# Performance work log

Measured on AMD Instinct MI355X. Metric: run time of the kernel, lower is better.

## Reference

```python
import jax, jax.numpy as jnp
import numpy as np

HIDDEN = 2048
N_HEADS = 16
N_KV_HEADS = 4
HEAD_DIM = 128
GROUPS = N_HEADS // N_KV_HEADS
MAX_SEQ = 2048
EPS = 1e-6
ROTARY_DIM = int(HEAD_DIM * 0.5)  # partial_rotary_factor = 0.5
ROPE_THETA = 10000.0


def _rms_norm(x, w):
    xf = x.astype(jnp.float32)
    normed = xf * jax.lax.rsqrt(jnp.mean(xf * xf, axis=-1, keepdims=True) + EPS)
    return (normed * (1.0 + w.astype(jnp.float32))).astype(x.dtype)


def _apply_rotary(x, cos, sin):
    half = x.shape[-1] // 2
    x1, x2 = x[..., :half], x[..., half:]
    return jnp.concatenate([x1 * cos - x2 * sin, x2 * cos + x1 * sin], axis=-1)


def setup_inputs() -> dict:
    key = jax.random.key(0)
    ks = jax.random.split(key, 6)
    s = 0.02
    return {
        "x": jax.random.normal(ks[0], (1, MAX_SEQ, HIDDEN), jnp.float32),
        "input_pos": jnp.arange(MAX_SEQ, dtype=jnp.int32),
        "wq": jax.random.normal(ks[1], (HIDDEN, N_HEADS * HEAD_DIM * 2), jnp.float32) * s,
        "wk": jax.random.normal(ks[2], (HIDDEN, N_KV_HEADS * HEAD_DIM), jnp.float32) * s,
        "wv": jax.random.normal(ks[3], (HIDDEN, N_KV_HEADS * HEAD_DIM), jnp.float32) * s,
        "wo": jax.random.normal(ks[4], (N_HEADS * HEAD_DIM, HIDDEN), jnp.float32) * s,
        "q_norm_w": jnp.zeros((HEAD_DIM,), jnp.float32),
        "k_norm_w": jnp.zeros((HEAD_DIM,), jnp.float32),
    }


def reference(x, input_pos, wq, wk, wv, wo, q_norm_w, k_norm_w):
    B, T, _ = x.shape
    dtype = x.dtype

    qg = (x @ wq).reshape(B, T, N_HEADS, HEAD_DIM * 2)
    q, gate = qg[..., :HEAD_DIM], qg[..., HEAD_DIM:]
    k = (x @ wk).reshape(B, T, N_KV_HEADS, HEAD_DIM)
    v = (x @ wv).reshape(B, T, N_KV_HEADS, HEAD_DIM)

    q = _rms_norm(q, q_norm_w)
    k = _rms_norm(k, k_norm_w)

    # partial RoPE on the first ROTARY_DIM channels of each head
    inv_freq = 1.0 / ROPE_THETA ** (
        jnp.arange(0, ROTARY_DIM, 2, dtype=jnp.float32) / ROTARY_DIM)
    freqs = jnp.outer(input_pos.astype(jnp.float32), inv_freq)  # [T, rd/2]
    cos = jnp.cos(freqs)[:, None, :]  # [T,1,rd/2] broadcast over heads
    sin = jnp.sin(freqs)[:, None, :]
    q = jnp.concatenate(
        [_apply_rotary(q[..., :ROTARY_DIM], cos, sin), q[..., ROTARY_DIM:]], axis=-1)
    k = jnp.concatenate(
        [_apply_rotary(k[..., :ROTARY_DIM], cos, sin), k[..., ROTARY_DIM:]], axis=-1)

    q = q.astype(dtype).transpose(0, 2, 1, 3)  # [B,H,T,D]
    k = k.astype(dtype).transpose(0, 2, 1, 3)  # [B,Hkv,T,D]
    v = v.transpose(0, 2, 1, 3)

    # KV-cache scatter update (cache starts at zeros)
    kc = jnp.zeros((1, N_KV_HEADS, MAX_SEQ, HEAD_DIM), dtype).at[:, :, input_pos].set(k)
    vc = jnp.zeros((1, N_KV_HEADS, MAX_SEQ, HEAD_DIM), dtype).at[:, :, input_pos].set(v)

    # GQA: group query heads instead of materializing repeated K/V
    qg_ = q.reshape(B, N_KV_HEADS, GROUPS, T, HEAD_DIM)
    scale = 1.0 / jnp.sqrt(jnp.asarray(HEAD_DIM, dtype))
    scores = jnp.einsum("bhgtd,bhsd->bhgts", qg_, kc) * scale  # [B,Hkv,G,T,S]

    mask = jnp.tril(jnp.ones((MAX_SEQ, MAX_SEQ), bool))[input_pos]  # [T,S]
    scores = jnp.where(mask[None, None, None], scores, jnp.finfo(scores.dtype).min)
    probs = jax.nn.softmax(scores, axis=-1)

    y = jnp.einsum("bhgts,bhsd->bhgtd", probs, vc)  # [B,Hkv,G,T,D]
    y = y.reshape(B, N_HEADS, T, HEAD_DIM).transpose(0, 2, 1, 3).reshape(B, T, -1)

    y = y * jax.nn.sigmoid(gate.reshape(B, T, -1))
    return y @ wo
```

## Files before the change

kernel.cpp:

```cpp
#include <hip/hip_runtime.h>
#include <cstdint>
#include <cmath>

using u16 = unsigned short;
typedef __attribute__((ext_vector_type(4))) short s16x4;
typedef __attribute__((ext_vector_type(8))) short s16x8;
typedef __attribute__((ext_vector_type(8))) __bf16 bf16x8;
typedef __attribute__((ext_vector_type(4))) float f32x4;

static __device__ __forceinline__ float b2f(u16 u) {
    unsigned int x = ((unsigned int)u) << 16;
    float f; __builtin_memcpy(&f, &x, 4); return f;
}
static __device__ __forceinline__ u16 f2b(float f) {
    unsigned int x; __builtin_memcpy(&x, &f, 4);
    x += 0x7FFFu + ((x >> 16) & 1u);
    return (u16)(x >> 16);
}
static __device__ __forceinline__ bf16x8 as_bf(s16x8 s) {
    return __builtin_bit_cast(bf16x8, s);
}

static __device__ __forceinline__ void stage16(const u16* g, u16* lds_base, int lane) {
#if __has_builtin(__builtin_amdgcn_global_load_lds)
    __builtin_amdgcn_global_load_lds((const __attribute__((address_space(1))) void*)g,
                                     (__attribute__((address_space(3))) void*)lds_base,
                                     16, 0, 0);
#else
    *(s16x8*)(lds_base + (size_t)lane * 8) = *(const s16x8*)g;
#endif
}

__global__ __launch_bounds__(256) void k_wtrans(const float* __restrict__ in,
                                                u16* __restrict__ out,
                                                int K, int N) {
    __shared__ u16 tile[64][72];
    int nb = blockIdx.x * 64, kb = blockIdx.y * 64;
    int tid = threadIdx.x;
    int kr = tid >> 2, c0 = (tid & 3) * 16;
#pragma unroll
    for (int i = 0; i < 4; ++i) {
        f32x4 v = *(const f32x4*)(in + (size_t)(kb + kr) * N + nb + c0 + i * 4);
        s16x4 b;
        for (int j = 0; j < 4; ++j) b[j] = (short)f2b(v[j]);
        *(s16x4*)&tile[kr][c0 + i * 4] = b;
    }
    __syncthreads();
    int nr = tid >> 2, k0 = (tid & 3) * 16;
    s16x8 v0, v1;
    for (int j = 0; j < 8; ++j) { v0[j] = (short)tile[k0 + j][nr]; v1[j] = (short)tile[k0 + 8 + j][nr]; }
    *(s16x8*)(out + (size_t)(nb + nr) * K + kb + k0) = v0;
    *(s16x8*)(out + (size_t)(nb + nr) * K + kb + k0 + 8) = v1;
}

__global__ __launch_bounds__(256) void k_xcvt(const float* __restrict__ in,
                                              u16* __restrict__ out, int n4) {
    int i = blockIdx.x * 256 + threadIdx.x;
    int stride = gridDim.x * 256;
    for (; i < n4; i += stride) {
        f32x4 v = ((const f32x4*)in)[i];
        s16x4 b;
        for (int j = 0; j < 4; ++j) b[j] = (short)f2b(v[j]);
        ((s16x4*)out)[i] = b;
    }
}

template <bool OUT_F32>
__global__ __launch_bounds__(256) void k_gemm_bt(const u16* __restrict__ A,
                                                 const u16* __restrict__ Bt,
                                                 void* __restrict__ Cv,
                                                 int M, int N, int K) {
    __shared__ u16 As[128 * 64];
    __shared__ u16 Bs[128 * 64];
    int nx = gridDim.x, nwg = nx * gridDim.y;
    int flat = blockIdx.y * nx + blockIdx.x;
    int q = nwg >> 3, r = nwg & 7;
    int xcd = flat & 7, idx = flat >> 3;
    int wgid = (xcd < r ? xcd * (q + 1) : r * (q + 1) + (xcd - r) * q) + idx;
    int bn = (wgid % nx) * 128, bm = (wgid / nx) * 128;

    int tid = threadIdx.x, wid = tid >> 6, lane = tid & 63;
    int l15 = lane & 15, g = lane >> 4;
    int wr = (wid >> 1) * 64, wc = (wid & 1) * 64;
    f32x4 acc[4][4];
    for (int i = 0; i < 4; ++i) for (int j = 0; j < 4; ++j) acc[i][j] = f32x4{0.f, 0.f, 0.f, 0.f};

    int srow = lane >> 3;
    int scol = ((lane & 7) * 8) ^ (srow << 3);
    const u16* pa = A + (size_t)(bm + srow) * K + scol;
    const u16* pb = Bt + (size_t)(bn + srow) * K + scol;

    for (int kb = 0; kb < K; kb += 64) {
        __syncthreads();
#pragma unroll
        for (int it = 0; it < 4; ++it) {
            int c = it * 4 + wid;
            stage16(pa + (size_t)(c * 8) * K + kb, &As[c * 512], lane);
            stage16(pb + (size_t)(c * 8) * K + kb, &Bs[c * 512], lane);
        }
        __syncthreads();
        int swz = (l15 & 7) << 4;
#pragma unroll
        for (int kk = 0; kk < 64; kk += 32) {
            bf16x8 af[4], bfr[4];
            for (int mi = 0; mi < 4; ++mi) {
                const char* rp = (const char*)As + (wr + mi * 16 + l15) * 128;
                af[mi] = as_bf(*(const s16x8*)(rp + ((kk * 2 + g * 16) ^ swz)));
            }
            for (int ni = 0; ni < 4; ++ni) {
                const char* rp = (const char*)Bs + (wc + ni * 16 + l15) * 128;
                bfr[ni] = as_bf(*(const s16x8*)(rp + ((kk * 2 + g * 16) ^ swz)));
            }
            for (int mi = 0; mi < 4; ++mi)
                for (int ni = 0; ni < 4; ++ni)
                    acc[mi][ni] = __builtin_amdgcn_mfma_f32_16x16x32_bf16(af[mi], bfr[ni], acc[mi][ni], 0, 0, 0);
        }
    }
    for (int mi = 0; mi < 4; ++mi)
        for (int ni = 0; ni < 4; ++ni) {
            int row = bm + wr + mi * 16 + g * 4;
            int col = bn + wc + ni * 16 + l15;
            for (int rr = 0; rr < 4; ++rr) {
                if (OUT_F32)
                    ((float*)Cv)[(size_t)(row + rr) * N + col] = acc[mi][ni][rr];
                else
                    ((u16*)Cv)[(size_t)(row + rr) * N + col] = f2b(acc[mi][ni][rr]);
            }
        }
}

__global__ __launch_bounds__(256) void k_normrope(u16* __restrict__ qkv,
                                                  const float* __restrict__ qw,
                                                  const float* __restrict__ kw,
                                                  const int* __restrict__ pos) {
    int t = blockIdx.x;
    int tid = threadIdx.x, w = tid >> 6, l = tid & 63;
    float fp = (float)pos[t];
    int j = l & 31;
    float invf = __expf(-(float)j * (9.210340371976184f / 32.f));
    float sv, cv;
    sincosf(fp * invf, &sv, &cv);
    for (int task = w; task < 20; task += 4) {
        u16* p; const float* ww;
        if (task < 16) { p = qkv + (size_t)t * 5120 + task * 256; ww = qw; }
        else           { p = qkv + (size_t)t * 5120 + 4096 + (task - 16) * 128; ww = kw; }
        float v0 = b2f(p[l]), v1 = b2f(p[l + 64]);
        float ss = v0 * v0 + v1 * v1;
        for (int m = 32; m; m >>= 1) ss += __shfl_xor(ss, m);
        float rn = rsqrtf(ss * (1.f / 128.f) + 1e-6f);
        float q0 = v0 * rn * (1.f + ww[l]);
        float q1 = v1 * rn * (1.f + ww[l + 64]);
        float other = __shfl_xor(q0, 32);
        float ro = (l < 32) ? (q0 * cv - other * sv) : (q0 * cv + other * sv);
        p[l] = f2b(ro);
        p[l + 64] = f2b(q1);
    }
}

__global__ __launch_bounds__(256) void k_vtrans(const u16* __restrict__ qkv,
                                                u16* __restrict__ vT) {
    __shared__ u16 tile[64][136];
    int tb = blockIdx.x * 64, kvh = blockIdx.y;
    int tid = threadIdx.x;
    int tr = tid >> 2, c0 = (tid & 3) * 32;
    const u16* src = qkv + (size_t)(tb + tr) * 5120 + 4608 + kvh * 128 + c0;
#pragma unroll
    for (int i = 0; i < 4; ++i)
        *(s16x8*)&tile[tr][c0 + i * 8] = *(const s16x8*)(src + i * 8);
    __syncthreads();
    int d = tid >> 1, t0 = (tid & 1) * 32;
    u16* dst = vT + ((size_t)kvh * 128 + d) * 2048 + tb + t0;
#pragma unroll
    for (int i = 0; i < 4; ++i) {
        s16x8 v;
        for (int j = 0; j < 8; ++j) v[j] = (short)tile[t0 + i * 8 + j][d];
        *(s16x8*)(dst + i * 8) = v;
    }
}

__global__ __launch_bounds__(256) void k_attn_split(const u16* __restrict__ qkv,
                                                    const u16* __restrict__ vT,
                                                    u16* __restrict__ po,
                                                    float* __restrict__ pl) {
    __shared__ u16 Kl[64 * 128];
    __shared__ u16 Vt[128][72];
    __shared__ u16 Pl[4][16][72];
    int head = blockIdx.y, kvh = head >> 2;
    int p = blockIdx.x >> 1, hf = blockIdx.x & 1;
    int tid = threadIdx.x, wid = tid >> 6, lane = tid & 63;
    int l15 = lane & 15, g = lane >> 4;

    for (int sub = 0; sub < 2; ++sub) {
        int qt = sub ? (31 - p) : p;
        int qb0 = qt * 64;
        int nk_all = qt + 1;
        int split = (nk_all + 1) >> 1;
        int ktb = hf ? split : 0;
        int kte = hf ? nk_all : split;

        bf16x8 qf[4];
        {
            const u16* qp = qkv + (size_t)(qb0 + wid * 16 + l15) * 5120 + head * 256 + g * 8;
            for (int c = 0; c < 4; ++c) qf[c] = as_bf(*(const s16x8*)(qp + c * 32));
        }
        f32x4 oacc[8];
        for (int nb = 0; nb < 8; ++nb) oacc[nb] = f32x4{0.f, 0.f, 0.f, 0.f};
        float lsum[4] = {0.f, 0.f, 0.f, 0.f};

        for (int kt = ktb; kt < kte; ++kt) {
            int k0 = kt * 64;
            __syncthreads();
            {
#pragma unroll
                for (int i = 0; i < 4; ++i) {
                    int c = (wid << 2) | i;
                    int srow = (c << 2) + (lane >> 4);
                    int bofs = (((lane & 15) << 4) ^ ((srow & 7) << 4));
                    const u16* gs = (const u16*)((const char*)(qkv + (size_t)(k0 + srow) * 5120
                                                               + 4096 + kvh * 128) + bofs);
                    stage16(gs, &Kl[c * 512], lane);
                }
                int vr = tid >> 1, vc0 = (tid & 1) * 32;
                const u16* vs = vT + ((size_t)kvh * 128 + vr) * 2048 + k0 + vc0;
#pragma unroll
                for (int c = 0; c < 4; ++c)
                    *(s16x8*)&Vt[vr][vc0 + 8 * c] = *(const s16x8*)(vs + 8 * c);
            }
            __syncthreads();

            f32x4 sc4[4];
            for (int h2 = 0; h2 < 4; ++h2) sc4[h2] = f32x4{0.f, 0.f, 0.f, 0.f};
            for (int h2 = 0; h2 < 4; ++h2) {
                int krow = h2 * 16 + l15;
                const char* kb_ = (const char*)Kl + krow * 256;
                int sw = (krow & 7) << 4;
                for (int c = 0; c < 4; ++c) {
                    bf16x8 kf = as_bf(*(const s16x8*)(kb_ + ((c * 64 + g * 16) ^ sw)));
                    sc4[h2] = __builtin_amdgcn_mfma_f32_16x16x32_bf16(qf[c], kf, sc4[h2], 0, 0, 0);
                }
            }
            const float scale = 0.08838834764831845f;
            for (int r = 0; r < 4; ++r) {
                int tq = qb0 + wid * 16 + g * 4 + r;
                float prs = 0.f;
                for (int h2 = 0; h2 < 4; ++h2) {
                    bool msk = (k0 + h2 * 16 + l15) > tq;
                    float pv = msk ? 0.f : __expf(sc4[h2][r] * scale);
                    prs += pv;
                    Pl[wid][g * 4 + r][h2 * 16 + l15] = f2b(pv);
                }
                lsum[r] += prs;
            }
            for (int kc = 0; kc < 2; ++kc) {
                bf16x8 pa = as_bf(*(const s16x8*)&Pl[wid][l15][kc * 32 + g * 8]);
                for (int nb = 0; nb < 8; ++nb) {
                    bf16x8 vb = as_bf(*(const s16x8*)&Vt[nb * 16 + l15][kc * 32 + g * 8]);
                    oacc[nb] = __builtin_amdgcn_mfma_f32_16x16x32_bf16(pa, vb, oacc[nb], 0, 0, 0);
                }
            }
        }
        u16* pob = po + (((size_t)hf * 16 + head) * 2048) * 128;
        float* plb = pl + ((size_t)hf * 16 + head) * 2048;
        for (int r = 0; r < 4; ++r) {
            float s = lsum[r];
            s += __shfl_xor(s, 1, 16); s += __shfl_xor(s, 2, 16);
            s += __shfl_xor(s, 4, 16); s += __shfl_xor(s, 8, 16);
            int row = qb0 + wid * 16 + g * 4 + r;
            if (l15 == 0) plb[row] = s;
            for (int nb = 0; nb < 8; ++nb)
                pob[(size_t)row * 128 + nb * 16 + l15] = f2b(oacc[nb][r]);
        }
    }
}

__global__ __launch_bounds__(256) void k_combine(const u16* __restrict__ po,
                                                 const float* __restrict__ pl,
                                                 const u16* __restrict__ qkv,
                                                 u16* __restrict__ yg) {
    int t = blockIdx.x;
    int tid = threadIdx.x;
    int h = tid >> 4, d0 = (tid & 15) * 8;
    const size_t base = ((size_t)h * 2048 + t) * 128 + d0;
    const size_t hofs = (size_t)16 * 2048 * 128;
    s16x8 a = *(const s16x8*)(po + base);
    s16x8 b = *(const s16x8*)(po + hofs + base);
    float l = pl[(size_t)h * 2048 + t] + pl[(size_t)16 * 2048 + (size_t)h * 2048 + t];
    float inv = 1.f / l;
    s16x8 o;
    for (int j = 0; j < 8; ++j) {
        float y = (b2f((u16)a[j]) + b2f((u16)b[j])) * inv;
        float gt = b2f(qkv[(size_t)t * 5120 + h * 256 + 128 + d0 + j]);
        o[j] = (short)f2b(y / (1.f + __expf(-gt)));
    }
    *(s16x8*)(yg + (size_t)t * 2048 + h * 128 + d0) = o;
}

extern "C" void kernel_launch(void* const* d_in, const int* in_sizes, int n_in,
                              void* d_out, int out_size, void* d_ws, size_t ws_size,
                              hipStream_t stream) {
    const float* x   = (const float*)d_in[0];
    const int*   pos = (const int*)d_in[1];
    const float* wq  = (const float*)d_in[2];
    const float* wk  = (const float*)d_in[3];
    const float* wv  = (const float*)d_in[4];
    const float* wo  = (const float*)d_in[5];
    const float* qnw = (const float*)d_in[6];
    const float* knw = (const float*)d_in[7];
    float* out = (float*)d_out;
    char* ws = (char*)d_ws;

    u16*   qkv   = (u16*)(ws + 0);
    u16*   woT   = (u16*)(ws + 20971520);
    u16*   wqkvT = (u16*)(ws + 29360128);
    u16*   xb    = (u16*)(ws + 50331648);
    u16*   vTb   = (u16*)(ws + 29360128);
    float* plb   = (float*)(ws + 31457280);
    u16*   pob   = (u16*)(ws + 31719424);
    u16*   ygb   = (u16*)(ws + 48496640);

    k_wtrans<<<dim3(64, 32), 256, 0, stream>>>(wq, wqkvT, 2048, 4096);
    k_wtrans<<<dim3(8, 32), 256, 0, stream>>>(wk, wqkvT + (size_t)4096 * 2048, 2048, 512);
    k_wtrans<<<dim3(8, 32), 256, 0, stream>>>(wv, wqkvT + (size_t)4608 * 2048, 2048, 512);
    k_wtrans<<<dim3(32, 32), 256, 0, stream>>>(wo, woT, 2048, 2048);
    k_xcvt<<<1024, 256, 0, stream>>>(x, xb, 2048 * 2048 / 4);

    k_gemm_bt<false><<<dim3(40, 16), 256, 0, stream>>>(xb, wqkvT, qkv, 2048, 5120, 2048);

    k_normrope<<<2048, 256, 0, stream>>>(qkv, qnw, knw, pos);
    k_vtrans<<<dim3(32, 4), 256, 0, stream>>>(qkv, vTb);

    k_attn_split<<<dim3(32, 16), 256, 0, stream>>>(qkv, vTb, pob, plb);
    k_combine<<<2048, 256, 0, stream>>>(pob, plb, qkv, ygb);

    k_gemm_bt<true><<<dim3(16, 16), 256, 0, stream>>>(ygb, woT, out, 2048, 2048, 2048);
}
```

Measured before the change: 190.5 us.

## Fuse norm+RoPE into QKV GEMM epilogue and combine+gate into output GEMM prologue

```diff
diff --git a/kernel.cpp b/kernel.cpp
--- a/kernel.cpp
+++ b/kernel.cpp
@@ -65,18 +65,25 @@
     }
 }
 
-template <bool OUT_F32>
+template <int EPI, bool COMBINE>
 __global__ __launch_bounds__(256) void k_gemm_bt(const u16* __restrict__ A,
                                                  const u16* __restrict__ Bt,
                                                  void* __restrict__ Cv,
-                                                 int M, int N, int K) {
-    __shared__ u16 As[128 * 64];
-    __shared__ u16 Bs[128 * 64];
+                                                 int M, int N, int K,
+                                                 const float* __restrict__ qnw,
+                                                 const float* __restrict__ knw,
+                                                 const int* __restrict__ pos,
+                                                 const u16* __restrict__ po,
+                                                 const float* __restrict__ pl,
+                                                 const u16* __restrict__ qkvg) {
+    __shared__ __align__(16) u16 lds[2 * 128 * 64];
+    u16* As = lds;
+    u16* Bs = lds + 128 * 64;
     int nx = gridDim.x, nwg = nx * gridDim.y;
     int flat = blockIdx.y * nx + blockIdx.x;
-    int q = nwg >> 3, r = nwg & 7;
+    int q8 = nwg >> 3, r8 = nwg & 7;
     int xcd = flat & 7, idx = flat >> 3;
-    int wgid = (xcd < r ? xcd * (q + 1) : r * (q + 1) + (xcd - r) * q) + idx;
+    int wgid = (xcd < r8 ? xcd * (q8 + 1) : r8 * (q8 + 1) + (xcd - r8) * q8) + idx;
     int bn = (wgid % nx) * 128, bm = (wgid / nx) * 128;
 
     int tid = threadIdx.x, wid = tid >> 6, lane = tid & 63;
@@ -87,15 +94,42 @@
 
     int srow = lane >> 3;
     int scol = ((lane & 7) * 8) ^ (srow << 3);
-    const u16* pa = A + (size_t)(bm + srow) * K + scol;
+    const u16* pa = COMBINE ? nullptr : (A + (size_t)(bm + srow) * K + scol);
     const u16* pb = Bt + (size_t)(bn + srow) * K + scol;
 
     for (int kb = 0; kb < K; kb += 64) {
         __syncthreads();
+        if constexpr (COMBINE) {
+            const size_t hofs = (size_t)16 * 2048 * 128;
+            int j = kb + scol;
+            int h = j >> 7, d0 = j & 127;
+#pragma unroll
+            for (int it = 0; it < 4; ++it) {
+                int c = it * 4 + wid;
+                int t = bm + c * 8 + srow;
+                size_t pbase = (((size_t)h * 2048 + t) << 7) + d0;
+                s16x8 a8 = *(const s16x8*)(po + pbase);
+                s16x8 b8 = *(const s16x8*)(po + hofs + pbase);
+                float linv = 1.f / (pl[h * 2048 + t] + pl[16 * 2048 + h * 2048 + t]);
+                s16x8 g8 = *(const s16x8*)(qkvg + (size_t)t * 5120 + h * 256 + 128 + d0);
+                s16x8 o;
+                for (int e = 0; e < 8; ++e) {
+                    float y = (b2f((u16)a8[e]) + b2f((u16)b8[e])) * linv;
+                    float gt = b2f((u16)g8[e]);
+                    o[e] = (short)f2b(y / (1.f + __expf(-gt)));
+                }
+                *(s16x8*)&As[c * 512 + lane * 8] = o;
+            }
+        } else {
+#pragma unroll
+            for (int it = 0; it < 4; ++it) {
+                int c = it * 4 + wid;
+                stage16(pa + (size_t)(c * 8) * K + kb, &As[c * 512], lane);
+            }
+        }
 #pragma unroll
         for (int it = 0; it < 4; ++it) {
             int c = it * 4 + wid;
-            stage16(pa + (size_t)(c * 8) * K + kb, &As[c * 512], lane);
             stage16(pb + (size_t)(c * 8) * K + kb, &Bs[c * 512], lane);
         }
         __syncthreads();
@@ -116,45 +150,68 @@
                     acc[mi][ni] = __builtin_amdgcn_mfma_f32_16x16x32_bf16(af[mi], bfr[ni], acc[mi][ni], 0, 0, 0);
         }
     }
+
+    if constexpr (EPI == 1) {
+        int blk = bn >> 7;
+        bool isq = (blk < 32) && !(blk & 1);
+        bool isk = (blk >= 32) && (blk < 36);
+        if (isq || isk) {
+            const float* w = isq ? qnw : knw;
+            float* sbuf = (float*)lds;
+            int half = wc >> 6;
+            __syncthreads();
+            for (int mi = 0; mi < 4; ++mi)
+                for (int rr = 0; rr < 4; ++rr) {
+                    float s = 0.f;
+                    for (int ni = 0; ni < 4; ++ni) { float v = acc[mi][ni][rr]; s += v * v; }
+                    s += __shfl_xor(s, 1, 16); s += __shfl_xor(s, 2, 16);
+                    s += __shfl_xor(s, 4, 16); s += __shfl_xor(s, 8, 16);
+                    if (l15 == 0) sbuf[half * 128 + wr + mi * 16 + g * 4 + rr] = s;
+                }
+            __syncthreads();
+            float invf0 = 0.f, invf1 = 0.f;
+            if (wc == 0) {
+                invf0 = __expf(-(float)l15 * (9.210340371976184f / 32.f));
+                invf1 = __expf(-(float)(l15 + 16) * (9.210340371976184f / 32.f));
+            }
+            for (int mi = 0; mi < 4; ++mi)
+                for (int rr = 0; rr < 4; ++rr) {
+                    int rl = wr + mi * 16 + g * 4 + rr;
+                    int t = bm + rl;
+                    float tot = sbuf[rl] + sbuf[128 + rl];
+                    float rn = rsqrtf(tot * (1.f / 128.f) + 1e-6f);
+                    float v[4];
+                    for (int ni = 0; ni < 4; ++ni)
+                        v[ni] = acc[mi][ni][rr] * rn * (1.f + w[wc + ni * 16 + l15]);
+                    if (wc == 0) {
+                        float fp = (float)pos[t];
+                        float s0, c0, s1, c1;
+                        sincosf(fp * invf0, &s0, &c0);
+                        sincosf(fp * invf1, &s1, &c1);
+                        float o0 = v[0] * c0 - v[2] * s0;
+                        float o1 = v[1] * c1 - v[3] * s1;
+                        float o2 = v[2] * c0 + v[0] * s0;
+                        float o3 = v[3] * c1 + v[1] * s1;
+                        v[0] = o0; v[1] = o1; v[2] = o2; v[3] = o3;
+                    }
+                    u16* Cp = (u16*)Cv + (size_t)t * N + bn + wc;
+                    for (int ni = 0; ni < 4; ++ni)
+                        Cp[ni * 16 + l15] = f2b(v[ni]);
+                }
+            return;
+        }
+    }
     for (int mi = 0; mi < 4; ++mi)
         for (int ni = 0; ni < 4; ++ni) {
             int row = bm + wr + mi * 16 + g * 4;
             int col = bn + wc + ni * 16 + l15;
             for (int rr = 0; rr < 4; ++rr) {
-                if (OUT_F32)
+                if (EPI == 2)
                     ((float*)Cv)[(size_t)(row + rr) * N + col] = acc[mi][ni][rr];
                 else
                     ((u16*)Cv)[(size_t)(row + rr) * N + col] = f2b(acc[mi][ni][rr]);
             }
         }
-}
-
-__global__ __launch_bounds__(256) void k_normrope(u16* __restrict__ qkv,
-                                                  const float* __restrict__ qw,
-                                                  const float* __restrict__ kw,
-                                                  const int* __restrict__ pos) {
-    int t = blockIdx.x;
-    int tid = threadIdx.x, w = tid >> 6, l = tid & 63;
-    float fp = (float)pos[t];
-    int j = l & 31;
-    float invf = __expf(-(float)j * (9.210340371976184f / 32.f));
-    float sv, cv;
-    sincosf(fp * invf, &sv, &cv);
-    for (int task = w; task < 20; task += 4) {
-        u16* p; const float* ww;
-        if (task < 16) { p = qkv + (size_t)t * 5120 + task * 256; ww = qw; }
-        else           { p = qkv + (size_t)t * 5120 + 4096 + (task - 16) * 128; ww = kw; }
-        float v0 = b2f(p[l]), v1 = b2f(p[l + 64]);
-        float ss = v0 * v0 + v1 * v1;
-        for (int m = 32; m; m >>= 1) ss += __shfl_xor(ss, m);
-        float rn = rsqrtf(ss * (1.f / 128.f) + 1e-6f);
-        float q0 = v0 * rn * (1.f + ww[l]);
-        float q1 = v1 * rn * (1.f + ww[l + 64]);
-        float other = __shfl_xor(q0, 32);
-        float ro = (l < 32) ? (q0 * cv - other * sv) : (q0 * cv + other * sv);
-        p[l] = f2b(ro);
-        p[l + 64] = f2b(q1);
-    }
 }
 
 __global__ __launch_bounds__(256) void k_vtrans(const u16* __restrict__ qkv,
@@ -271,28 +328,6 @@
                 pob[(size_t)row * 128 + nb * 16 + l15] = f2b(oacc[nb][r]);
         }
     }
-}
-
-__global__ __launch_bounds__(256) void k_combine(const u16* __restrict__ po,
-                                                 const float* __restrict__ pl,
-                                                 const u16* __restrict__ qkv,
-                                                 u16* __restrict__ yg) {
-    int t = blockIdx.x;
-    int tid = threadIdx.x;
-    int h = tid >> 4, d0 = (tid & 15) * 8;
-    const size_t base = ((size_t)h * 2048 + t) * 128 + d0;
-    const size_t hofs = (size_t)16 * 2048 * 128;
-    s16x8 a = *(const s16x8*)(po + base);
-    s16x8 b = *(const s16x8*)(po + hofs + base);
-    float l = pl[(size_t)h * 2048 + t] + pl[(size_t)16 * 2048 + (size_t)h * 2048 + t];
-    float inv = 1.f / l;
-    s16x8 o;
-    for (int j = 0; j < 8; ++j) {
-        float y = (b2f((u16)a[j]) + b2f((u16)b[j])) * inv;
-        float gt = b2f(qkv[(size_t)t * 5120 + h * 256 + 128 + d0 + j]);
-        o[j] = (short)f2b(y / (1.f + __expf(-gt)));
-    }
-    *(s16x8*)(yg + (size_t)t * 2048 + h * 128 + d0) = o;
 }
 
 extern "C" void kernel_launch(void* const* d_in, const int* in_sizes, int n_in,
@@ -316,7 +351,6 @@
     u16*   vTb   = (u16*)(ws + 29360128);
     float* plb   = (float*)(ws + 31457280);
     u16*   pob   = (u16*)(ws + 31719424);
-    u16*   ygb   = (u16*)(ws + 48496640);
 
     k_wtrans<<<dim3(64, 32), 256, 0, stream>>>(wq, wqkvT, 2048, 4096);
     k_wtrans<<<dim3(8, 32), 256, 0, stream>>>(wk, wqkvT + (size_t)4096 * 2048, 2048, 512);
@@ -324,13 +358,13 @@
     k_wtrans<<<dim3(32, 32), 256, 0, stream>>>(wo, woT, 2048, 2048);
     k_xcvt<<<1024, 256, 0, stream>>>(x, xb, 2048 * 2048 / 4);
 
-    k_gemm_bt<false><<<dim3(40, 16), 256, 0, stream>>>(xb, wqkvT, qkv, 2048, 5120, 2048);
-
-    k_normrope<<<2048, 256, 0, stream>>>(qkv, qnw, knw, pos);
+    k_gemm_bt<1, false><<<dim3(40, 16), 256, 0, stream>>>(xb, wqkvT, qkv, 2048, 5120, 2048,
+                                                          qnw, knw, pos, nullptr, nullptr, nullptr);
+
     k_vtrans<<<dim3(32, 4), 256, 0, stream>>>(qkv, vTb);
 
     k_attn_split<<<dim3(32, 16), 256, 0, stream>>>(qkv, vTb, pob, plb);
-    k_combine<<<2048, 256, 0, stream>>>(pob, plb, qkv, ygb);
-
-    k_gemm_bt<true><<<dim3(16, 16), 256, 0, stream>>>(ygb, woT, out, 2048, 2048, 2048);
-}
+
+    k_gemm_bt<2, true><<<dim3(16, 16), 256, 0, stream>>>(nullptr, woT, out, 2048, 2048, 2048,
+                                                         nullptr, nullptr, nullptr, pob, plb, qkv);
+}
```

New measurement: 293.4 us. +54.0%, slower.

## Split attention KV range three ways and merge small prep launches

Applied to the files above, without the earlier changes.

```diff
diff --git a/kernel.cpp b/kernel.cpp
--- a/kernel.cpp
+++ b/kernel.cpp
@@ -31,16 +31,25 @@
 #endif
 }
 
-__global__ __launch_bounds__(256) void k_wtrans(const float* __restrict__ in,
-                                                u16* __restrict__ out,
-                                                int K, int N) {
+__global__ __launch_bounds__(256) void k_wtransAll(const float* __restrict__ wq,
+                                                   const float* __restrict__ wk,
+                                                   const float* __restrict__ wv,
+                                                   const float* __restrict__ wo,
+                                                   u16* __restrict__ wqkvT,
+                                                   u16* __restrict__ woT) {
     __shared__ u16 tile[64][72];
-    int nb = blockIdx.x * 64, kb = blockIdx.y * 64;
+    int tx = blockIdx.x;
+    const float* src; int N, nb, base; u16* dst;
+    if (tx < 64)      { src = wq; N = 4096; nb = tx * 64;        base = tx * 64;               dst = wqkvT; }
+    else if (tx < 72) { src = wk; N = 512;  nb = (tx - 64) * 64; base = 4096 + (tx - 64) * 64; dst = wqkvT; }
+    else if (tx < 80) { src = wv; N = 512;  nb = (tx - 72) * 64; base = 4608 + (tx - 72) * 64; dst = wqkvT; }
+    else              { src = wo; N = 2048; nb = (tx - 80) * 64; base = (tx - 80) * 64;        dst = woT; }
+    int kb = blockIdx.y * 64;
     int tid = threadIdx.x;
     int kr = tid >> 2, c0 = (tid & 3) * 16;
 #pragma unroll
     for (int i = 0; i < 4; ++i) {
-        f32x4 v = *(const f32x4*)(in + (size_t)(kb + kr) * N + nb + c0 + i * 4);
+        f32x4 v = *(const f32x4*)(src + (size_t)(kb + kr) * N + nb + c0 + i * 4);
         s16x4 b;
         for (int j = 0; j < 4; ++j) b[j] = (short)f2b(v[j]);
         *(s16x4*)&tile[kr][c0 + i * 4] = b;
@@ -49,8 +58,8 @@
     int nr = tid >> 2, k0 = (tid & 3) * 16;
     s16x8 v0, v1;
     for (int j = 0; j < 8; ++j) { v0[j] = (short)tile[k0 + j][nr]; v1[j] = (short)tile[k0 + 8 + j][nr]; }
-    *(s16x8*)(out + (size_t)(nb + nr) * K + kb + k0) = v0;
-    *(s16x8*)(out + (size_t)(nb + nr) * K + kb + k0 + 8) = v1;
+    *(s16x8*)(dst + (size_t)(base + nr) * 2048 + kb + k0) = v0;
+    *(s16x8*)(dst + (size_t)(base + nr) * 2048 + kb + k0 + 8) = v1;
 }
 
 __global__ __launch_bounds__(256) void k_xcvt(const float* __restrict__ in,
@@ -74,9 +83,9 @@
     __shared__ u16 Bs[128 * 64];
     int nx = gridDim.x, nwg = nx * gridDim.y;
     int flat = blockIdx.y * nx + blockIdx.x;
-    int q = nwg >> 3, r = nwg & 7;
+    int q8 = nwg >> 3, r8 = nwg & 7;
     int xcd = flat & 7, idx = flat >> 3;
-    int wgid = (xcd < r ? xcd * (q + 1) : r * (q + 1) + (xcd - r) * q) + idx;
+    int wgid = (xcd < r8 ? xcd * (q8 + 1) : r8 * (q8 + 1) + (xcd - r8) * q8) + idx;
     int bn = (wgid % nx) * 128, bm = (wgid / nx) * 128;
 
     int tid = threadIdx.x, wid = tid >> 6, lane = tid & 63;
@@ -129,52 +138,53 @@
         }
 }
 
-__global__ __launch_bounds__(256) void k_normrope(u16* __restrict__ qkv,
-                                                  const float* __restrict__ qw,
-                                                  const float* __restrict__ kw,
-                                                  const int* __restrict__ pos) {
-    int t = blockIdx.x;
-    int tid = threadIdx.x, w = tid >> 6, l = tid & 63;
-    float fp = (float)pos[t];
-    int j = l & 31;
-    float invf = __expf(-(float)j * (9.210340371976184f / 32.f));
-    float sv, cv;
-    sincosf(fp * invf, &sv, &cv);
-    for (int task = w; task < 20; task += 4) {
-        u16* p; const float* ww;
-        if (task < 16) { p = qkv + (size_t)t * 5120 + task * 256; ww = qw; }
-        else           { p = qkv + (size_t)t * 5120 + 4096 + (task - 16) * 128; ww = kw; }
-        float v0 = b2f(p[l]), v1 = b2f(p[l + 64]);
-        float ss = v0 * v0 + v1 * v1;
-        for (int m = 32; m; m >>= 1) ss += __shfl_xor(ss, m);
-        float rn = rsqrtf(ss * (1.f / 128.f) + 1e-6f);
-        float q0 = v0 * rn * (1.f + ww[l]);
-        float q1 = v1 * rn * (1.f + ww[l + 64]);
-        float other = __shfl_xor(q0, 32);
-        float ro = (l < 32) ? (q0 * cv - other * sv) : (q0 * cv + other * sv);
-        p[l] = f2b(ro);
-        p[l + 64] = f2b(q1);
-    }
-}
-
-__global__ __launch_bounds__(256) void k_vtrans(const u16* __restrict__ qkv,
-                                                u16* __restrict__ vT) {
+__global__ __launch_bounds__(256) void k_prep_attn(u16* __restrict__ qkv,
+                                                   const float* __restrict__ qw,
+                                                   const float* __restrict__ kw,
+                                                   const int* __restrict__ pos,
+                                                   u16* __restrict__ vT) {
     __shared__ u16 tile[64][136];
-    int tb = blockIdx.x * 64, kvh = blockIdx.y;
+    int bid = blockIdx.x;
     int tid = threadIdx.x;
-    int tr = tid >> 2, c0 = (tid & 3) * 32;
-    const u16* src = qkv + (size_t)(tb + tr) * 5120 + 4608 + kvh * 128 + c0;
-#pragma unroll
-    for (int i = 0; i < 4; ++i)
-        *(s16x8*)&tile[tr][c0 + i * 8] = *(const s16x8*)(src + i * 8);
-    __syncthreads();
-    int d = tid >> 1, t0 = (tid & 1) * 32;
-    u16* dst = vT + ((size_t)kvh * 128 + d) * 2048 + tb + t0;
-#pragma unroll
-    for (int i = 0; i < 4; ++i) {
-        s16x8 v;
-        for (int j = 0; j < 8; ++j) v[j] = (short)tile[t0 + i * 8 + j][d];
-        *(s16x8*)(dst + i * 8) = v;
+    if (bid < 2048) {
+        int t = bid, w = tid >> 6, l = tid & 63;
+        float fp = (float)pos[t];
+        int j = l & 31;
+        float invf = __expf(-(float)j * (9.210340371976184f / 32.f));
+        float sv, cv;
+        sincosf(fp * invf, &sv, &cv);
+        for (int task = w; task < 20; task += 4) {
+            u16* p; const float* ww;
+            if (task < 16) { p = qkv + (size_t)t * 5120 + task * 256; ww = qw; }
+            else           { p = qkv + (size_t)t * 5120 + 4096 + (task - 16) * 128; ww = kw; }
+            float v0 = b2f(p[l]), v1 = b2f(p[l + 64]);
+            float ss = v0 * v0 + v1 * v1;
+            for (int m = 32; m; m >>= 1) ss += __shfl_xor(ss, m);
+            float rn = rsqrtf(ss * (1.f / 128.f) + 1e-6f);
+            float q0 = v0 * rn * (1.f + ww[l]);
+            float q1 = v1 * rn * (1.f + ww[l + 64]);
+            float other = __shfl_xor(q0, 32);
+            float ro = (l < 32) ? (q0 * cv - other * sv) : (q0 * cv + other * sv);
+            p[l] = f2b(ro);
+            p[l + 64] = f2b(q1);
+        }
+    } else {
+        int r = bid - 2048;
+        int tb = (r & 31) * 64, kvh = r >> 5;
+        int tr = tid >> 2, c0 = (tid & 3) * 32;
+        const u16* src = qkv + (size_t)(tb + tr) * 5120 + 4608 + kvh * 128 + c0;
+#pragma unroll
+        for (int i = 0; i < 4; ++i)
+            *(s16x8*)&tile[tr][c0 + i * 8] = *(const s16x8*)(src + i * 8);
+        __syncthreads();
+        int d = tid >> 1, t0 = (tid & 1) * 32;
+        u16* dst = vT + ((size_t)kvh * 128 + d) * 2048 + tb + t0;
+#pragma unroll
+        for (int i = 0; i < 4; ++i) {
+            s16x8 v;
+            for (int j = 0; j < 8; ++j) v[j] = (short)tile[t0 + i * 8 + j][d];
+            *(s16x8*)(dst + i * 8) = v;
+        }
     }
 }
 
@@ -186,7 +196,7 @@
     __shared__ u16 Vt[128][72];
     __shared__ u16 Pl[4][16][72];
     int head = blockIdx.y, kvh = head >> 2;
-    int p = blockIdx.x >> 1, hf = blockIdx.x & 1;
+    int p = blockIdx.x / 3, hf = blockIdx.x % 3;
     int tid = threadIdx.x, wid = tid >> 6, lane = tid & 63;
     int l15 = lane & 15, g = lane >> 4;
 
@@ -194,9 +204,8 @@
         int qt = sub ? (31 - p) : p;
         int qb0 = qt * 64;
         int nk_all = qt + 1;
-        int split = (nk_all + 1) >> 1;
-        int ktb = hf ? split : 0;
-        int kte = hf ? nk_all : split;
+        int ktb = (hf * nk_all) / 3;
+        int kte = ((hf + 1) * nk_all) / 3;
 
         bf16x8 qf[4];
         {
@@ -259,8 +268,8 @@
                 }
             }
         }
-        u16* pob = po + (((size_t)hf * 16 + head) * 2048) * 128;
-        float* plb = pl + ((size_t)hf * 16 + head) * 2048;
+        u16* pob = po + (size_t)hf * (2048 * 2048);
+        float* plb = pl + hf * (16 * 2048) + head * 2048;
         for (int r = 0; r < 4; ++r) {
             float s = lsum[r];
             s += __shfl_xor(s, 1, 16); s += __shfl_xor(s, 2, 16);
@@ -268,31 +277,32 @@
             int row = qb0 + wid * 16 + g * 4 + r;
             if (l15 == 0) plb[row] = s;
             for (int nb = 0; nb < 8; ++nb)
-                pob[(size_t)row * 128 + nb * 16 + l15] = f2b(oacc[nb][r]);
-        }
-    }
-}
-
-__global__ __launch_bounds__(256) void k_combine(const u16* __restrict__ po,
+                pob[(size_t)row * 2048 + head * 128 + nb * 16 + l15] = f2b(oacc[nb][r]);
+        }
+    }
+}
+
+__global__ __launch_bounds__(256) void k_combine(u16* __restrict__ po,
                                                  const float* __restrict__ pl,
-                                                 const u16* __restrict__ qkv,
-                                                 u16* __restrict__ yg) {
+                                                 const u16* __restrict__ qkv) {
     int t = blockIdx.x;
     int tid = threadIdx.x;
     int h = tid >> 4, d0 = (tid & 15) * 8;
-    const size_t base = ((size_t)h * 2048 + t) * 128 + d0;
-    const size_t hofs = (size_t)16 * 2048 * 128;
+    const size_t S = (size_t)2048 * 2048;
+    const size_t base = (size_t)t * 2048 + h * 128 + d0;
     s16x8 a = *(const s16x8*)(po + base);
-    s16x8 b = *(const s16x8*)(po + hofs + base);
-    float l = pl[(size_t)h * 2048 + t] + pl[(size_t)16 * 2048 + (size_t)h * 2048 + t];
+    s16x8 b = *(const s16x8*)(po + S + base);
+    s16x8 c = *(const s16x8*)(po + 2 * S + base);
+    int li = h * 2048 + t;
+    float l = pl[li] + pl[16 * 2048 + li] + pl[32 * 2048 + li];
     float inv = 1.f / l;
     s16x8 o;
     for (int j = 0; j < 8; ++j) {
-        float y = (b2f((u16)a[j]) + b2f((u16)b[j])) * inv;
+        float y = (b2f((u16)a[j]) + b2f((u16)b[j]) + b2f((u16)c[j])) * inv;
         float gt = b2f(qkv[(size_t)t * 5120 + h * 256 + 128 + d0 + j]);
         o[j] = (short)f2b(y / (1.f + __expf(-gt)));
     }
-    *(s16x8*)(yg + (size_t)t * 2048 + h * 128 + d0) = o;
+    *(s16x8*)(po + base) = o;
 }
 
 extern "C" void kernel_launch(void* const* d_in, const int* in_sizes, int n_in,
@@ -314,23 +324,18 @@
     u16*   wqkvT = (u16*)(ws + 29360128);
     u16*   xb    = (u16*)(ws + 50331648);
     u16*   vTb   = (u16*)(ws + 29360128);
-    float* plb   = (float*)(ws + 31457280);
-    u16*   pob   = (u16*)(ws + 31719424);
-    u16*   ygb   = (u16*)(ws + 48496640);
-
-    k_wtrans<<<dim3(64, 32), 256, 0, stream>>>(wq, wqkvT, 2048, 4096);
-    k_wtrans<<<dim3(8, 32), 256, 0, stream>>>(wk, wqkvT + (size_t)4096 * 2048, 2048, 512);
-    k_wtrans<<<dim3(8, 32), 256, 0, stream>>>(wv, wqkvT + (size_t)4608 * 2048, 2048, 512);
-    k_wtrans<<<dim3(32, 32), 256, 0, stream>>>(wo, woT, 2048, 2048);
+    u16*   pob   = (u16*)(ws + 31457280);
+    float* plb   = (float*)(ws + 56623104);
+
+    k_wtransAll<<<dim3(112, 32), 256, 0, stream>>>(wq, wk, wv, wo, wqkvT, woT);
     k_xcvt<<<1024, 256, 0, stream>>>(x, xb, 2048 * 2048 / 4);
 
     k_gemm_bt<false><<<dim3(40, 16), 256, 0, stream>>>(xb, wqkvT, qkv, 2048, 5120, 2048);
 
-    k_normrope<<<2048, 256, 0, stream>>>(qkv, qnw, knw, pos);
-    k_vtrans<<<dim3(32, 4), 256, 0, stream>>>(qkv, vTb);
-
-    k_attn_split<<<dim3(32, 16), 256, 0, stream>>>(qkv, vTb, pob, plb);
-    k_combine<<<2048, 256, 0, stream>>>(pob, plb, qkv, ygb);
-
-    k_gemm_bt<true><<<dim3(16, 16), 256, 0, stream>>>(ygb, woT, out, 2048, 2048, 2048);
-}
+    k_prep_attn<<<2176, 256, 0, stream>>>(qkv, qnw, knw, pos, vTb);
+
+    k_attn_split<<<dim3(48, 16), 256, 0, stream>>>(qkv, vTb, pob, plb);
+    k_combine<<<2048, 256, 0, stream>>>(pob, plb, qkv);
+
+    k_gemm_bt<true><<<dim3(16, 16), 256, 0, stream>>>(pob, woT, out, 2048, 2048, 2048);
+}
```

New measurement: 178.9 us. -6.1%, faster.
